# Optimization experiments

Hardware: AMD Instinct MI355X
Metric: run time of the kernel (lower is better)

The kernel has to match this reference:

```python
import jax, jax.numpy as jnp
import numpy as np

UP = 2  # upsample2d default up factor

def create_lowpass_kernel(weights):
    # CreateLowpassKernel(weights, inplace=False): convolve with [1,1], outer product, normalize
    k = np.convolve(np.asarray(weights, dtype=np.float64), [1.0, 1.0]).reshape(1, -1)
    k = k.T @ k
    return jnp.asarray(k / k.sum(), dtype=jnp.float32)

def setup_inputs() -> dict:
    key = jax.random.key(0)
    x = jax.random.normal(key, (16, 128, 128, 128), dtype=jnp.float32)
    kernel = create_lowpass_kernel([1.0, 3.0, 3.0, 1.0])  # 5x5
    return {"x": x, "kernel": kernel}

def reference(x, kernel):
    # upfirdn2d.upsample2d(x, f, up=2): zero-insertion upsample + pad + FIR filter, gain=up^2.
    N, C, H, W = x.shape
    fh, fw = kernel.shape
    # upsample2d padding: p0=(f+up-1)//2, p1=(f-up)//2 on the zero-inserted grid (H*up long,
    # with up-1 trailing zeros). lax lhs_dilation yields (H-1)*up+1, so add up-1 to right pad.
    p0 = (fh + UP - 1) // 2
    p1 = (fh - UP) // 2 + (UP - 1)
    # gain = up*up; upfirdn flips the filter (correlation -> true convolution);
    # lax.conv_general_dilated computes correlation, so flip explicitly (kernel is symmetric anyway).
    f = (kernel * (UP * UP))[::-1, ::-1]
    w = jnp.tile(f[None, None], (C, 1, 1, 1))  # depthwise: (C,1,fh,fw)
    return jax.lax.conv_general_dilated(
        x, w,
        window_strides=(1, 1),
        padding=((p0, p1), (p0, p1)),
        lhs_dilation=(UP, UP),
        dimension_numbers=("NCHW", "OIHW", "NCHW"),
        feature_group_count=C,
    )
```

## Files before the change

### kernel.cpp

```cpp
#include <hip/hip_runtime.h>


#define IH 128
#define IW 128
#define OW 256

__global__ __launch_bounds__(256) void up2_wave(
    const float* __restrict__ x, float* __restrict__ out)
{
    int gtid = blockIdx.x * 256 + threadIdx.x;
    int wave = gtid >> 6;
    int lane = gtid & 63;
    int p  = wave >> 4;
    int rg = wave & 15;
    int m0 = rg * 8;

    const float* xp = x + (size_t)p * (IH * IW);
    float* op = out + (size_t)p * (OW * OW);

    int c0 = lane * 2;

    float a0,a1,a2,a3, b0,b1,b2,b3;

#define LOADROW(ry, r0, r1, r2, r3)                                   \
    {                                                                 \
        float2 v;                                                     \
        if ((ry) >= 0 && (ry) < IH)          \
            v = *reinterpret_cast<const float2*>(xp + (ry) * IW + c0);\
        else                                                          \
            v = make_float2(0.f, 0.f);                                \
        r1 = v.x; r2 = v.y;                                           \
        r0 = __shfl(v.y, lane - 1);                     \
        r3 = __shfl(v.x, lane + 1);                     \
        if (lane == 0)  r0 = 0.f;                                     \
        if (lane == 63) r3 = 0.f;                                     \
    }

    LOADROW(m0 - 1, a0, a1, a2, a3)
    LOADROW(m0,     b0, b1, b2, b3)

#pragma unroll
    for (int i = 0; i < 8; ++i) {
        int m = m0 + i;
        float n0, n1, n2, n3;
        LOADROW(m + 1, n0, n1, n2, n3)

        float ve0 = 0.5f*(a0+b0), ve1 = 0.5f*(a1+b1);
        float ve2 = 0.5f*(a2+b2), ve3 = 0.5f*(a3+b3);
        float vo0 = 0.125f*a0 + 0.75f*b0 + 0.125f*n0;
        float vo1 = 0.125f*a1 + 0.75f*b1 + 0.125f*n1;
        float vo2 = 0.125f*a2 + 0.75f*b2 + 0.125f*n2;
        float vo3 = 0.125f*a3 + 0.75f*b3 + 0.125f*n3;

        float4 re, ro;
        re.x = 0.5f*(ve0+ve1);
        re.y = 0.125f*ve0 + 0.75f*ve1 + 0.125f*ve2;
        re.z = 0.5f*(ve1+ve2);
        re.w = 0.125f*ve1 + 0.75f*ve2 + 0.125f*ve3;
        ro.x = 0.5f*(vo0+vo1);
        ro.y = 0.125f*vo0 + 0.75f*vo1 + 0.125f*vo2;
        ro.z = 0.5f*(vo1+vo2);
        ro.w = 0.125f*vo1 + 0.75f*vo2 + 0.125f*vo3;

        float* dst = op + (size_t)(2*m) * OW + 4*lane;
        *reinterpret_cast<float4*>(dst)      = re;
        *reinterpret_cast<float4*>(dst + OW) = ro;

        a0=b0; a1=b1; a2=b2; a3=b3;
        b0=n0; b1=n1; b2=n2; b3=n3;
    }
#undef LOADROW
}

extern "C" void kernel_launch(void* const* d_in, const int* in_sizes, int n_in,
                              void* d_out, int out_size, void* d_ws, size_t ws_size,
                              hipStream_t stream)
{
    const float* x = (const float*)d_in[0];
    float* out = (float*)d_out;
    int nplanes = in_sizes[0] / (IH * IW);
    int waves = nplanes * 16;
    int total_threads = waves * 64;
    int blocks = (total_threads + 255) / 256;
    up2_wave<<<blocks, 256, 0, stream>>>(x, out);
}
```

Baseline: 128.0 us.

## Use longer row strips, prefetch next row, and nontemporal output stores

Each wave now handles 32 input rows instead of 8, so the halo rows re-read at strip edges are amortized over more work and the grid has a quarter as many waves. The load of row m+2 is issued one iteration early, hiding global-load latency behind the current row's arithmetic and shuffles. Output float4 stores become nontemporal stores to reduce cache pollution from the 128 MiB write stream. The trade-off is fewer waves for latency hiding (2048 × 4 = 8192 waves) and a partially unrolled loop.

```diff
diff --git a/kernel.cpp b/kernel.cpp
--- a/kernel.cpp
+++ b/kernel.cpp
@@ -4,6 +4,9 @@
 #define IH 128
 #define IW 128
 #define OW 256
+#define RSTRIP 32
+
+typedef float f32x4 __attribute__((ext_vector_type(4)));
 
 __global__ __launch_bounds__(256) void up2_wave(
     const float* __restrict__ x, float* __restrict__ out)
@@ -11,39 +14,49 @@
     int gtid = blockIdx.x * 256 + threadIdx.x;
     int wave = gtid >> 6;
     int lane = gtid & 63;
-    int p  = wave >> 4;
-    int rg = wave & 15;
-    int m0 = rg * 8;
+    int p  = wave >> 2;
+    int sg = wave & 3;
+    int m0 = sg * RSTRIP;
 
     const float* xp = x + (size_t)p * (IH * IW);
     float* op = out + (size_t)p * (OW * OW);
-
     int c0 = lane * 2;
 
-    float a0,a1,a2,a3, b0,b1,b2,b3;
-
-#define LOADROW(ry, r0, r1, r2, r3)                                   \
-    {                                                                 \
-        float2 v;                                                     \
-        if ((ry) >= 0 && (ry) < IH)          \
-            v = *reinterpret_cast<const float2*>(xp + (ry) * IW + c0);\
-        else                                                          \
-            v = make_float2(0.f, 0.f);                                \
-        r1 = v.x; r2 = v.y;                                           \
-        r0 = __shfl(v.y, lane - 1);                     \
-        r3 = __shfl(v.x, lane + 1);                     \
-        if (lane == 0)  r0 = 0.f;                                     \
-        if (lane == 63) r3 = 0.f;                                     \
+#define RAWLOAD(ry, v)                                                 \
+    {                                                                  \
+        if ((ry) >= 0 && (ry) < IH)                  \
+            v = *reinterpret_cast<const float2*>(xp + (ry) * IW + c0); \
+        else                                                           \
+            v = make_float2(0.f, 0.f);                                 \
     }
 
-    LOADROW(m0 - 1, a0, a1, a2, a3)
-    LOADROW(m0,     b0, b1, b2, b3)
+#define SHUF(v, r0, r1, r2, r3)                  \
+    {                                            \
+        r1 = v.x; r2 = v.y;                      \
+        r0 = __shfl(v.y, lane - 1);              \
+        r3 = __shfl(v.x, lane + 1);              \
+        if (lane == 0)  r0 = 0.f;                \
+        if (lane == 63) r3 = 0.f;                \
+    }
 
-#pragma unroll
-    for (int i = 0; i < 8; ++i) {
+    float2 vA, vB, vC;
+    RAWLOAD(m0 - 1, vA)
+    RAWLOAD(m0,     vB)
+    RAWLOAD(m0 + 1, vC)
+
+    float a0,a1,a2,a3, b0,b1,b2,b3;
+    SHUF(vA, a0, a1, a2, a3)
+    SHUF(vB, b0, b1, b2, b3)
+
+#pragma unroll 4
+    for (int i = 0; i < RSTRIP; ++i) {
         int m = m0 + i;
+
+        float2 vD;
+        RAWLOAD(m + 2, vD)
+
         float n0, n1, n2, n3;
-        LOADROW(m + 1, n0, n1, n2, n3)
+        SHUF(vC, n0, n1, n2, n3)
 
         float ve0 = 0.5f*(a0+b0), ve1 = 0.5f*(a1+b1);
         float ve2 = 0.5f*(a2+b2), ve3 = 0.5f*(a3+b3);
@@ -52,7 +65,7 @@
         float vo2 = 0.125f*a2 + 0.75f*b2 + 0.125f*n2;
         float vo3 = 0.125f*a3 + 0.75f*b3 + 0.125f*n3;
 
-        float4 re, ro;
+        f32x4 re, ro;
         re.x = 0.5f*(ve0+ve1);
         re.y = 0.125f*ve0 + 0.75f*ve1 + 0.125f*ve2;
         re.z = 0.5f*(ve1+ve2);
@@ -63,13 +76,15 @@
         ro.w = 0.125f*vo1 + 0.75f*vo2 + 0.125f*vo3;
 
         float* dst = op + (size_t)(2*m) * OW + 4*lane;
-        *reinterpret_cast<float4*>(dst)      = re;
-        *reinterpret_cast<float4*>(dst + OW) = ro;
+        __builtin_nontemporal_store(re, reinterpret_cast<f32x4*>(dst));
+        __builtin_nontemporal_store(ro, reinterpret_cast<f32x4*>(dst + OW));
 
         a0=b0; a1=b1; a2=b2; a3=b3;
         b0=n0; b1=n1; b2=n2; b3=n3;
+        vC = vD;
     }
-#undef LOADROW
+#undef RAWLOAD
+#undef SHUF
 }
 
 extern "C" void kernel_launch(void* const* d_in, const int* in_sizes, int n_in,
@@ -79,7 +94,7 @@
     const float* x = (const float*)d_in[0];
     float* out = (float*)d_out;
     int nplanes = in_sizes[0] / (IH * IW);
-    int waves = nplanes * 16;
+    int waves = nplanes * (IH / RSTRIP);
     int total_threads = waves * 64;
     int blocks = (total_threads + 255) / 256;
     up2_wave<<<blocks, 256, 0, stream>>>(x, out);
```

New measurement: 104.6 us. 18.3% less time.
